# Optimization experiments

Hardware: AMD Instinct MI355X
Metric: run time of the kernel (lower is better)

The kernel has to match this reference:

```python
import jax, jax.numpy as jnp
import numpy as np

B, S, D, H = 4, 2048, 1024, 16
HD = D // H
SCALE = HD ** -0.5


def setup_inputs() -> dict:
    key = jax.random.key(0)
    ks = jax.random.split(key, 5)
    std = D ** -0.5
    return {
        "x": jax.random.normal(ks[0], (B, S, D), jnp.float32),
        "wq": jax.random.normal(ks[1], (D, D), jnp.float32) * std,
        "bq": jnp.zeros((D,), jnp.float32),
        "wk": jax.random.normal(ks[2], (D, D), jnp.float32) * std,
        "bk": jnp.zeros((D,), jnp.float32),
        "wv": jax.random.normal(ks[3], (D, D), jnp.float32) * std,
        "bv": jnp.zeros((D,), jnp.float32),
        "wo": jax.random.normal(ks[4], (D, D), jnp.float32) * std,
        "bo": jnp.zeros((D,), jnp.float32),
    }


def reference(x, wq, bq, wk, bk, wv, bv, wo, bo):
    # projections; weights stored as [in, out] so y = x @ w + b
    q = (x @ wq + bq).reshape(B, S, H, HD).transpose(0, 2, 1, 3)  # [B,H,S,HD]
    k = (x @ wk + bk).reshape(B, S, H, HD).transpose(0, 2, 1, 3)
    v = (x @ wv + bv).reshape(B, S, H, HD).transpose(0, 2, 1, 3)
    attn = jnp.einsum("bhqd,bhkd->bhqk", q, k) * SCALE  # [B,H,S,S]
    attn = jax.nn.softmax(attn, axis=-1)
    out = jnp.einsum("bhqk,bhkd->bhqd", attn, v)  # [B,H,S,HD]
    out = out.transpose(0, 2, 1, 3).reshape(B, S, D)
    return out @ wo + bo
```

## Files before the change

### kernel.cpp

```cpp
#include <hip/hip_runtime.h>
#include <stdint.h>


typedef __attribute__((ext_vector_type(8))) short bf16x8;
typedef __attribute__((ext_vector_type(4))) short bf16x4;
typedef __attribute__((ext_vector_type(4))) float f32x4;
typedef __attribute__((ext_vector_type(16))) float f32x16;
typedef __attribute__((ext_vector_type(4))) int i32x4;
typedef unsigned short u16;
typedef unsigned int u32;

#define AS1 __attribute__((address_space(1)))
#define AS3 __attribute__((address_space(3)))

#define SCALE_L2E 0.18033688011112042f

__device__ __forceinline__ void gld_lds16(const void* g, void* l) {
  __builtin_amdgcn_global_load_lds((const AS1 void*)g, (AS3 void*)l, 16, 0, 0);
}

__device__ __forceinline__ u16 f2bf(float f) {
  u32 x = __builtin_bit_cast(u32, f);
  x += 0x7fff + ((x >> 16) & 1);
  return (u16)(x >> 16);
}

__device__ __forceinline__ u16 f2bf_fast(float a) {
#if __has_builtin(__builtin_amdgcn_cvt_pk_bf16_f32)
  auto v = __builtin_amdgcn_cvt_pk_bf16_f32(a, a);
  return (u16)(__builtin_bit_cast(u32, v) & 0xffffu);
#else
  return f2bf(a);
#endif
}

__device__ __forceinline__ u32 pk2(float a, float b) {
#if __has_builtin(__builtin_amdgcn_cvt_pk_bf16_f32)
  return __builtin_bit_cast(u32, __builtin_amdgcn_cvt_pk_bf16_f32(a, b));
#else
  return (u32)f2bf(a) | ((u32)f2bf(b) << 16);
#endif
}

__device__ __forceinline__ float exp2_fast(float x) {
#if __has_builtin(__builtin_amdgcn_exp2f)
  return __builtin_amdgcn_exp2f(x);
#else
  return exp2f(x);
#endif
}

__device__ __forceinline__ f32x16 zero16() {
  f32x16 z;
#pragma unroll
  for (int i = 0; i < 16; ++i) z[i] = 0.f;
  return z;
}

__global__ __launch_bounds__(256) void convert_x(const float* __restrict__ x,
                                                 u16* __restrict__ xb) {
  int i = (blockIdx.x * 256 + threadIdx.x) * 4;
  float4 v = *(const float4*)(x + i);
  ushort4 o;
  o.x = f2bf(v.x); o.y = f2bf(v.y); o.z = f2bf(v.z); o.w = f2bf(v.w);
  *(ushort4*)(xb + i) = o;
}

__global__ __launch_bounds__(256) void pack_weights(
    const float* __restrict__ wq, const float* __restrict__ wk,
    const float* __restrict__ wv, const float* __restrict__ wo,
    u16* __restrict__ wt_qkv, u16* __restrict__ wt_o) {
  __shared__ float tile[64][65];
  int mat = blockIdx.z;
  const float* src = (mat == 0) ? wq : (mat == 1) ? wk : (mat == 2) ? wv : wo;
  int k0 = blockIdx.y * 64, j0 = blockIdx.x * 64;
  int t = threadIdx.x;
  int lr = t >> 6;
  int lc = t & 63;
#pragma unroll
  for (int it = 0; it < 16; ++it) {
    int r = it * 4 + lr;
    tile[r][lc] = src[(size_t)(k0 + r) * 1024 + j0 + lc];
  }
  __syncthreads();
  u16* dst = (mat == 3) ? wt_o : (wt_qkv + (size_t)mat * 1024 * 1024);
#pragma unroll
  for (int it = 0; it < 16; ++it) {
    int nl = it * 4 + lr;
    float v = tile[lc][nl];
    if (mat == 0) v *= SCALE_L2E;
    dst[(size_t)(j0 + nl) * 1024 + k0 + lc] = f2bf(v);
  }
}

__global__ __launch_bounds__(512, 4) void gemm_qkv(
    const u16* __restrict__ A, const u16* __restrict__ Bt,
    const float* __restrict__ bias0, const float* __restrict__ bias1,
    const float* __restrict__ bias2,
    u16* __restrict__ outQ, u16* __restrict__ outK, u16* __restrict__ outV) {
  __shared__ u16 lA[2][128 * 32];
  __shared__ u16 lB[2][256 * 32];
  int tid = threadIdx.x;
  int wave = tid >> 6, lane = tid & 63;
  int wr = wave >> 2, wc = wave & 3;

  int bid = blockIdx.x;
  int xcd = bid & 7, j = bid >> 3;
  int m0 = (xcd * 8 + (j & 7)) * 128;
  int n0 = (j >> 3) * 256;

  f32x4 acc[4][4];
#pragma unroll
  for (int fm = 0; fm < 4; ++fm)
#pragma unroll
    for (int fn = 0; fn < 4; ++fn) acc[fm][fn] = f32x4{0.f, 0.f, 0.f, 0.f};

  int srow = lane >> 2;
  int schunk = ((lane & 3) ^ ((lane >> 3) & 3)) * 8;
  int fr = lane & 15;
  int rpos = (((lane >> 4) ^ ((fr >> 1) & 3))) * 8;

  const u16* Asrc = A + (size_t)(m0 + wave * 16 + srow) * 1024 + schunk;
  const u16* Bsrc0 = Bt + (size_t)(n0 + wave * 32 + srow) * 1024 + schunk;
  const u16* Bsrc1 = Bsrc0 + (size_t)16 * 1024;

  gld_lds16(Asrc, &lA[0][wave * 16 * 32]);
  gld_lds16(Bsrc0, &lB[0][wave * 32 * 32]);
  gld_lds16(Bsrc1, &lB[0][(wave * 32 + 16) * 32]);
  __syncthreads();

  int cur = 0;
  for (int kt = 0; kt < 32; ++kt) {
    if (kt < 31) {
      int k1 = (kt + 1) * 32;
      gld_lds16(Asrc + k1, &lA[cur ^ 1][wave * 16 * 32]);
      gld_lds16(Bsrc0 + k1, &lB[cur ^ 1][wave * 32 * 32]);
      gld_lds16(Bsrc1 + k1, &lB[cur ^ 1][(wave * 32 + 16) * 32]);
    }
    bf16x8 af[4], bfv[4];
#pragma unroll
    for (int fm = 0; fm < 4; ++fm)
      af[fm] = *(const bf16x8*)(&lA[cur][(wr * 64 + fm * 16 + fr) * 32 + rpos]);
#pragma unroll
    for (int fn = 0; fn < 4; ++fn)
      bfv[fn] = *(const bf16x8*)(&lB[cur][(wc * 64 + fn * 16 + fr) * 32 + rpos]);
#pragma unroll
    for (int fm = 0; fm < 4; ++fm)
#pragma unroll
      for (int fn = 0; fn < 4; ++fn)
        acc[fm][fn] = __builtin_amdgcn_mfma_f32_16x16x32_bf16(
            af[fm], bfv[fn], acc[fm][fn], 0, 0, 0);
    __syncthreads();
    cur ^= 1;
  }

  int mat = n0 >> 10;
  const float* bp = (mat == 0) ? bias0 : (mat == 1) ? bias1 : bias2;
  int rb0 = m0 + wr * 64 + (lane >> 4) * 4;
  int jb = (n0 & 1023) + wc * 64;
#pragma unroll
  for (int fn = 0; fn < 4; ++fn) {
    int jj = jb + fn * 16 + fr;
    float bv = bp[jj];
    if (mat == 0) bv *= SCALE_L2E;
    if (mat == 2) {
      int h = jj >> 6, hd = jj & 63;
#pragma unroll
      for (int fm = 0; fm < 4; ++fm) {
        int row0 = rb0 + fm * 16;
        int b = row0 >> 11, s = row0 & 2047;
        int ci = s >> 6, sl = s & 63;
        int slice = sl >> 4, srem = sl & 15;
        size_t off = (size_t)(b * 16 + h) * 131072 + ci * 4096 + slice * 1024
                   + ((srem >> 2) & 1) * 512 + hd * 8 + (srem >> 3) * 4;
        ushort4 pk;
        pk.x = f2bf_fast(acc[fm][fn][0] + bv);
        pk.y = f2bf_fast(acc[fm][fn][1] + bv);
        pk.z = f2bf_fast(acc[fm][fn][2] + bv);
        pk.w = f2bf_fast(acc[fm][fn][3] + bv);
        *(ushort4*)(outV + off) = pk;
      }
    } else {
      u16* base = (mat == 0) ? outQ : outK;
#pragma unroll
      for (int fm = 0; fm < 4; ++fm)
#pragma unroll
        for (int rr = 0; rr < 4; ++rr)
          base[(size_t)(rb0 + fm * 16 + rr) * 1024 + jj] =
              f2bf_fast(acc[fm][fn][rr] + bv);
    }
  }
}

template <int MODE>
__global__ __launch_bounds__(256, 3) void gemm_bt(
    const u16* __restrict__ A, const u16* __restrict__ Bt,
    const float* __restrict__ bias0, const float* __restrict__ bias1,
    const float* __restrict__ bias2,
    void* __restrict__ out0v, void* __restrict__ out1v, void* __restrict__ out2v) {
  __shared__ u16 lA[128 * 32];
  __shared__ u16 lB[128 * 32];
  const int K = 1024;
  int tid = threadIdx.x;
  int wave = tid >> 6, lane = tid & 63;

  int bid = blockIdx.x;
  int n0 = (bid & 7) * 128;
  int m0 = (bid >> 3) * 128;
  int wm = (wave & 1) * 64, wn = (wave >> 1) * 64;

  f32x4 acc[4][4];
#pragma unroll
  for (int i = 0; i < 4; ++i)
#pragma unroll
    for (int jj = 0; jj < 4; ++jj) acc[i][jj] = f32x4{0.f, 0.f, 0.f, 0.f};

  int srow = lane >> 2;
  int scol = (lane & 3) * 8;

  for (int k0 = 0; k0 < K; k0 += 32) {
#pragma unroll
    for (int c = 0; c < 2; ++c) {
      int rbase = wave * 32 + c * 16;
      gld_lds16(A + (size_t)(m0 + rbase + srow) * K + k0 + scol, lA + rbase * 32);
      gld_lds16(Bt + (size_t)(n0 + rbase + srow) * K + k0 + scol, lB + rbase * 32);
    }
    __syncthreads();
    bf16x8 af[4], bfr[4];
#pragma unroll
    for (int mt = 0; mt < 4; ++mt)
      af[mt] = *(const bf16x8*)(lA + (wm + mt * 16 + (lane & 15)) * 32 + (lane >> 4) * 8);
#pragma unroll
    for (int nt = 0; nt < 4; ++nt)
      bfr[nt] = *(const bf16x8*)(lB + (wn + nt * 16 + (lane & 15)) * 32 + (lane >> 4) * 8);
#pragma unroll
    for (int mt = 0; mt < 4; ++mt)
#pragma unroll
      for (int nt = 0; nt < 4; ++nt)
        acc[mt][nt] = __builtin_amdgcn_mfma_f32_16x16x32_bf16(af[mt], bfr[nt], acc[mt][nt], 0, 0, 0);
    __syncthreads();
  }

  int rbase0 = m0 + wm + (lane >> 4) * 4;
  int cbase = n0 + wn + (lane & 15);
#pragma unroll
  for (int nt = 0; nt < 4; ++nt) {
    int col = cbase + nt * 16;
    float bv = bias0[col];
    float* o = (float*)out0v;
#pragma unroll
    for (int mt = 0; mt < 4; ++mt)
#pragma unroll
      for (int r = 0; r < 4; ++r) {
        int row = rbase0 + mt * 16 + r;
        o[(size_t)row * 1024 + col] = acc[mt][nt][r] + bv;
      }
  }
}

__global__ __launch_bounds__(512, 2) void flash_attn(
    const u16* __restrict__ Q, const u16* __restrict__ Kb,
    const u16* __restrict__ Vg, u16* __restrict__ ctx) {
  __shared__ u16 lK[2][64 * 32];
  __shared__ u16 lV[4096];
  int tid = threadIdx.x, wave = tid >> 6, lane = tid & 63;

  int F = blockIdx.x;
  int xcd = F & 7, idx = F >> 3;
  int bh = xcd * 8 + (idx >> 2);
  int q0 = (idx & 3) * 512;
  int b = bh >> 4, h = bh & 15;
  const u16* Qp = Q + (size_t)b * 2048 * 1024 + h * 64;
  const u16* Kp = Kb + (size_t)b * 2048 * 1024 + h * 64;
  const u16* Vp = Vg + (size_t)bh * 131072;

  int ql = lane & 31;
  int hi = lane >> 5;

  bf16x8 qf[2][4];
#pragma unroll
  for (int qt = 0; qt < 2; ++qt) {
    const u16* qrow = Qp + (size_t)(q0 + wave * 64 + qt * 32 + ql) * 1024;
#pragma unroll
    for (int kk = 0; kk < 4; ++kk)
      qf[qt][kk] = *(const bf16x8*)(qrow + kk * 16 + hi * 8);
  }

  float lsum[2] = {0.f, 0.f};
  f32x16 o[2][2];
#pragma unroll
  for (int qt = 0; qt < 2; ++qt)
#pragma unroll
    for (int dh = 0; dh < 2; ++dh) o[qt][dh] = zero16();

  int srow = lane >> 2;
  int schunk = (((lane & 3) ^ ((lane >> 3) & 3)) * 8);
  int kk_w = wave & 1;
  int rb = wave >> 1;
  int stg_row = rb * 16 + srow;
  int rkey = ((lane & 15) >> 1) & 3;

  const u16* gK = Kp + (size_t)stg_row * 1024 + kk_w * 32 + schunk;
  const u16* gV = Vp + wave * 512 + lane * 8;
  u16* wK = lK[kk_w] + rb * 512 + lane * 8;
  u16* wV = lV + wave * 512 + lane * 8;

  i32x4 ldK = *(const i32x4*)gK;
  i32x4 ldV = *(const i32x4*)gV;
  *(i32x4*)wK = ldK;
  *(i32x4*)wV = ldV;
  __syncthreads();

  for (int s0 = 0; s0 < 2048; s0 += 64) {
    bool more = (s0 + 64 < 2048);
    if (more) {
      ldK = *(const i32x4*)(gK + (size_t)(s0 + 64) * 1024);
      ldV = *(const i32x4*)(gV + (size_t)(s0 + 64) * 64);
    }

#pragma unroll
    for (int sb = 0; sb < 2; ++sb) {
      bf16x8 kf[4];
      int krb = (sb * 32 + ql) * 32;
#pragma unroll
      for (int kk = 0; kk < 4; ++kk)
        kf[kk] = *(const bf16x8*)(lK[kk >> 1] + krb + ((((kk & 1) << 1) | hi) ^ rkey) * 8);

      f32x16 sa0 = zero16(), sa1 = zero16();
#pragma unroll
      for (int kk = 0; kk < 4; ++kk) {
        sa0 = __builtin_amdgcn_mfma_f32_32x32x16_bf16(kf[kk], qf[0][kk], sa0, 0, 0, 0);
        sa1 = __builtin_amdgcn_mfma_f32_32x32x16_bf16(kf[kk], qf[1][kk], sa1, 0, 0, 0);
      }

      bf16x8 pu[2][2];
#pragma unroll
      for (int qt = 0; qt < 2; ++qt) {
        float p[16];
#pragma unroll
        for (int r = 0; r < 16; ++r)
          p[r] = exp2_fast(qt == 0 ? sa0[r] : sa1[r]);
        float a0 = (p[0] + p[1]) + (p[2] + p[3]);
        float a1 = (p[4] + p[5]) + (p[6] + p[7]);
        float a2 = (p[8] + p[9]) + (p[10] + p[11]);
        float a3 = (p[12] + p[13]) + (p[14] + p[15]);
        lsum[qt] += (a0 + a1) + (a2 + a3);
#pragma unroll
        for (int ss = 0; ss < 2; ++ss) {
          union { u32 w[4]; bf16x8 v; } pk_;
          pk_.w[0] = pk2(p[8 * ss + 0], p[8 * ss + 1]);
          pk_.w[1] = pk2(p[8 * ss + 2], p[8 * ss + 3]);
          pk_.w[2] = pk2(p[8 * ss + 4], p[8 * ss + 5]);
          pk_.w[3] = pk2(p[8 * ss + 6], p[8 * ss + 7]);
          pu[qt][ss] = pk_.v;
        }
      }

#pragma unroll
      for (int ss = 0; ss < 2; ++ss) {
        int vbase = (sb * 2 + ss) * 1024 + hi * 512 + ql * 8;
#pragma unroll
        for (int dh = 0; dh < 2; ++dh) {
          bf16x8 vf = *(const bf16x8*)(lV + vbase + dh * 256);
          o[0][dh] = __builtin_amdgcn_mfma_f32_32x32x16_bf16(vf, pu[0][ss], o[0][dh], 0, 0, 0);
          o[1][dh] = __builtin_amdgcn_mfma_f32_32x32x16_bf16(vf, pu[1][ss], o[1][dh], 0, 0, 0);
        }
      }
    }

    __syncthreads();
    if (more) {
      *(i32x4*)wK = ldK;
      *(i32x4*)wV = ldV;
    }
    __syncthreads();
  }

#pragma unroll
  for (int qt = 0; qt < 2; ++qt) {
    float rs = lsum[qt] + __shfl_xor(lsum[qt], 32);
    float inv = 1.0f / fmaxf(rs, 1e-30f);
    int q = q0 + wave * 64 + qt * 32 + ql;
    size_t rowbase = ((size_t)(b * 2048 + q) * 16 + h) * 64;
#pragma unroll
    for (int dh = 0; dh < 2; ++dh)
#pragma unroll
      for (int rr = 0; rr < 4; ++rr) {
        ushort4 pk;
        pk.x = f2bf_fast(o[qt][dh][4 * rr + 0] * inv);
        pk.y = f2bf_fast(o[qt][dh][4 * rr + 1] * inv);
        pk.z = f2bf_fast(o[qt][dh][4 * rr + 2] * inv);
        pk.w = f2bf_fast(o[qt][dh][4 * rr + 3] * inv);
        *(ushort4*)(ctx + rowbase + dh * 32 + rr * 8 + hi * 4) = pk;
      }
  }
}

extern "C" void kernel_launch(void* const* d_in, const int* in_sizes, int n_in,
                              void* d_out, int out_size, void* d_ws, size_t ws_size,
                              hipStream_t stream) {
  const float* x  = (const float*)d_in[0];
  const float* wq = (const float*)d_in[1];
  const float* bq = (const float*)d_in[2];
  const float* wk = (const float*)d_in[3];
  const float* bk = (const float*)d_in[4];
  const float* wv = (const float*)d_in[5];
  const float* bv = (const float*)d_in[6];
  const float* wo = (const float*)d_in[7];
  const float* bo = (const float*)d_in[8];

  u16* ws = (u16*)d_ws;
  u16* xb     = ws;
  u16* wt_qkv = xb + (size_t)8192 * 1024;
  u16* wt_o   = wt_qkv + (size_t)3072 * 1024;
  u16* Qb     = wt_o + (size_t)1024 * 1024;
  u16* Kbuf   = Qb + (size_t)8192 * 1024;
  u16* Vgb    = Kbuf + (size_t)8192 * 1024;
  u16* ctx    = Vgb + (size_t)8192 * 1024;

  convert_x<<<8192, 256, 0, stream>>>(x, xb);
  pack_weights<<<dim3(16, 16, 4), 256, 0, stream>>>(wq, wk, wv, wo, wt_qkv, wt_o);
  gemm_qkv<<<768, 512, 0, stream>>>(xb, wt_qkv, bq, bk, bv, Qb, Kbuf, Vgb);
  flash_attn<<<256, 512, 0, stream>>>(Qb, Kbuf, Vgb, ctx);
  gemm_bt<1><<<512, 256, 0, stream>>>(ctx, wt_o, bo, nullptr, nullptr,
                                      d_out, nullptr, nullptr);
}
```

Before: 279.7 us.

## Triple-buffer QKV GEMM LDS loads with partial vmcnt waits

The QKV projection GEMM moves from double to triple buffering in LDS and prefetches two K-tiles ahead. It waits only until the older tile's loads complete (vmcnt(3)) instead of a full __syncthreads drain. It also raises wave priority around the MFMA block. This is meant to hide global-to-LDS latency better, at the cost of 50% more LDS per block, which may reduce occupancy under launch_bounds(512,4).

```diff
diff --git a/kernel.cpp b/kernel.cpp
--- a/kernel.cpp
+++ b/kernel.cpp
@@ -98,8 +98,8 @@
     const float* __restrict__ bias0, const float* __restrict__ bias1,
     const float* __restrict__ bias2,
     u16* __restrict__ outQ, u16* __restrict__ outK, u16* __restrict__ outV) {
-  __shared__ u16 lA[2][128 * 32];
-  __shared__ u16 lB[2][256 * 32];
+  __shared__ u16 lA[3][128 * 32];
+  __shared__ u16 lB[3][256 * 32];
   int tid = threadIdx.x;
   int wave = tid >> 6, lane = tid & 63;
   int wr = wave >> 2, wc = wave & 3;
@@ -127,31 +127,45 @@
   gld_lds16(Asrc, &lA[0][wave * 16 * 32]);
   gld_lds16(Bsrc0, &lB[0][wave * 32 * 32]);
   gld_lds16(Bsrc1, &lB[0][(wave * 32 + 16) * 32]);
-  __syncthreads();
-
-  int cur = 0;
+  gld_lds16(Asrc + 32, &lA[1][wave * 16 * 32]);
+  gld_lds16(Bsrc0 + 32, &lB[1][wave * 32 * 32]);
+  gld_lds16(Bsrc1 + 32, &lB[1][(wave * 32 + 16) * 32]);
+  asm volatile("s_waitcnt vmcnt(3)" ::: "memory");
+  __builtin_amdgcn_s_barrier();
+  asm volatile("" ::: "memory");
+
+  int bR = 0;
   for (int kt = 0; kt < 32; ++kt) {
-    if (kt < 31) {
-      int k1 = (kt + 1) * 32;
-      gld_lds16(Asrc + k1, &lA[cur ^ 1][wave * 16 * 32]);
-      gld_lds16(Bsrc0 + k1, &lB[cur ^ 1][wave * 32 * 32]);
-      gld_lds16(Bsrc1 + k1, &lB[cur ^ 1][(wave * 32 + 16) * 32]);
+    int bS = bR + 2; if (bS >= 3) bS -= 3;
+    if (kt + 2 < 32) {
+      int k1 = (kt + 2) * 32;
+      gld_lds16(Asrc + k1, &lA[bS][wave * 16 * 32]);
+      gld_lds16(Bsrc0 + k1, &lB[bS][wave * 32 * 32]);
+      gld_lds16(Bsrc1 + k1, &lB[bS][(wave * 32 + 16) * 32]);
     }
     bf16x8 af[4], bfv[4];
 #pragma unroll
     for (int fm = 0; fm < 4; ++fm)
-      af[fm] = *(const bf16x8*)(&lA[cur][(wr * 64 + fm * 16 + fr) * 32 + rpos]);
+      af[fm] = *(const bf16x8*)(&lA[bR][(wr * 64 + fm * 16 + fr) * 32 + rpos]);
 #pragma unroll
     for (int fn = 0; fn < 4; ++fn)
-      bfv[fn] = *(const bf16x8*)(&lB[cur][(wc * 64 + fn * 16 + fr) * 32 + rpos]);
+      bfv[fn] = *(const bf16x8*)(&lB[bR][(wc * 64 + fn * 16 + fr) * 32 + rpos]);
+    __builtin_amdgcn_s_setprio(1);
 #pragma unroll
     for (int fm = 0; fm < 4; ++fm)
 #pragma unroll
       for (int fn = 0; fn < 4; ++fn)
         acc[fm][fn] = __builtin_amdgcn_mfma_f32_16x16x32_bf16(
             af[fm], bfv[fn], acc[fm][fn], 0, 0, 0);
-    __syncthreads();
-    cur ^= 1;
+    __builtin_amdgcn_s_setprio(0);
+    if (kt + 2 < 32) {
+      asm volatile("s_waitcnt vmcnt(3)" ::: "memory");
+    } else {
+      asm volatile("s_waitcnt vmcnt(0)" ::: "memory");
+    }
+    __builtin_amdgcn_s_barrier();
+    asm volatile("" ::: "memory");
+    bR = (bR == 2) ? 0 : bR + 1;
   }
 
   int mat = n0 >> 10;
```

Result: no change. 278.9 us (-0.3%).
